# Optimization experiments

Measured on AMD Instinct MI355X. Metric: run time of the kernel, lower is better.

Reference implementation:

```python
import jax, jax.numpy as jnp
import numpy as np

N_KNOTS = 8
LATENT = 16
DEGREE = 3


def _de_boor(x, t, c, p):
    # x: arbitrary-shape query points; t: (n_knots+6,) padded knots; c: (n_knots+2,) control points
    k = jnp.digitize(x, t) - 1  # interval index per element (binary search gather)
    d = [c[k + (j - p)] for j in range(p + 1)]
    for r in range(1, p + 1):
        for j in range(p, r - 1, -1):
            t_lo = t[k + (j - p)]
            t_hi = t[k + (j + 1 - r)]
            alpha = (x - t_lo) / (t_hi - t_lo)
            d[j] = (1.0 - alpha) * d[j - 1] + alpha * d[j]
    return d[p]


def setup_inputs() -> dict:
    key = jax.random.key(0)
    ks = jax.random.split(key, 8)
    # |k| grid normalized to fftfreq range: values in [0, sqrt(3)]
    x = jax.random.uniform(ks[0], (256, 256, 256), dtype=jnp.float32) * 1.7320508
    a = jax.random.uniform(ks[1], (1,), dtype=jnp.float32)  # scale factor in (0,1)
    inv = 1.0 / np.sqrt(LATENT).astype(np.float32)
    W1 = jax.random.normal(ks[2], (1, LATENT), jnp.float32)
    b1 = jnp.zeros((LATENT,), jnp.float32)
    W2 = jax.random.normal(ks[3], (LATENT, LATENT), jnp.float32) * inv
    b2 = jnp.zeros((LATENT,), jnp.float32)
    Ww = jax.random.normal(ks[4], (LATENT, N_KNOTS + 1), jnp.float32) * inv
    bw = jnp.zeros((N_KNOTS + 1,), jnp.float32)
    Wk = jax.random.normal(ks[5], (LATENT, N_KNOTS - 1), jnp.float32) * inv
    bk = jnp.zeros((N_KNOTS - 1,), jnp.float32)
    return {"x": x, "a": a, "W1": W1, "b1": b1, "W2": W2, "b2": b2,
            "Ww": Ww, "bw": bw, "Wk": Wk, "bk": bk}


def reference(x, a, W1, b1, W2, b2, Ww, bw, Wk, bk):
    # tiny MLP on scalar a -> spline weights w and knot increments k
    net = jnp.sin(a @ W1 + b1)           # (LATENT,)
    net = jnp.sin(net @ W2 + b2)         # (LATENT,)
    w = net @ Ww + bw                    # (N_KNOTS+1,)
    kk = net @ Wk + bk                   # (N_KNOTS-1,)
    kk = jnp.concatenate([jnp.zeros((1,), x.dtype), jnp.cumsum(jax.nn.softmax(kk))])  # (N_KNOTS,), monotone in [0,1]
    w = jnp.concatenate([jnp.zeros((1,), x.dtype), w])                                 # (N_KNOTS+2,)
    ak = jnp.concatenate([jnp.zeros((3,), x.dtype), kk, jnp.ones((3,), x.dtype)])      # padded knots
    xq = jnp.clip(x / jnp.sqrt(jnp.asarray(3.0, x.dtype)), 0.0, 1.0 - 0.0001)
    return _de_boor(xq, ak, w, DEGREE)
```

## Files before the change

kernel.cpp:

```cpp
#include <hip/hip_runtime.h>
#include <math.h>

typedef float f4 __attribute__((ext_vector_type(4)));

__device__ __forceinline__ float eval_one(float xv,
                                          float c1, float c2, float c3,
                                          float k1, float k2, float k3,
                                          float k4, float k5, float k6,
                                          float e1, float e2, float e3,
                                          float e4, float e5, float e6)
{
    const float xq = fminf(fmaxf(xv * 0.57735026918962576f, 0.0f), 0.9999f);
    float acc = xq * fmaf(fmaf(c3, xq, c2), xq, c1);
    float r;
    r = fmaxf(xq - k1, 0.f); acc = fmaf(e1 * r, r * r, acc);
    r = fmaxf(xq - k2, 0.f); acc = fmaf(e2 * r, r * r, acc);
    r = fmaxf(xq - k3, 0.f); acc = fmaf(e3 * r, r * r, acc);
    r = fmaxf(xq - k4, 0.f); acc = fmaf(e4 * r, r * r, acc);
    r = fmaxf(xq - k5, 0.f); acc = fmaf(e5 * r, r * r, acc);
    r = fmaxf(xq - k6, 0.f); acc = fmaf(e6 * r, r * r, acc);
    return acc;
}

__global__ __launch_bounds__(256) void nsf_fused2_kernel(
    const float* __restrict__ x,
    const float* __restrict__ a,
    const float* __restrict__ W1, const float* __restrict__ b1,
    const float* __restrict__ W2, const float* __restrict__ b2,
    const float* __restrict__ Ww, const float* __restrict__ bw,
    const float* __restrict__ Wk, const float* __restrict__ bk,
    float* __restrict__ out, int n)
{
    const int n4 = n >> 2;
    const int gid = blockIdx.x * blockDim.x + threadIdx.x;
    const int stride = gridDim.x * blockDim.x;
    const f4* __restrict__ x4 = reinterpret_cast<const f4*>(x);
    f4* __restrict__ o4 = reinterpret_cast<f4*>(out);

    const int j16 = threadIdx.x & 15;

    const float av  = a[0];
    const float w1v = W1[j16];
    const float b1v = b1[j16];
    const float b2v = b2[j16];
    float w2l[16];
#pragma unroll
    for (int i = 0; i < 16; ++i) w2l[i] = W2[i * 16 + j16];
    const bool isw = (j16 < 9);
    const float* hW = isw ? (Ww + j16) : (Wk + (j16 - 9));
    const int hs = isw ? 9 : 7;
    const float hbv = isw ? bw[j16] : bk[j16 - 9];
    float hl[16];
#pragma unroll
    for (int i = 0; i < 16; ++i) hl[i] = hW[i * hs];

    f4 v[8];
#pragma unroll
    for (int it = 0; it < 8; ++it) {
        const int idx = gid + it * stride;
        if (idx < n4) v[it] = __builtin_nontemporal_load(x4 + idx);
    }

    const float n1own = __sinf(fmaf(av, w1v, b1v));
    float s2 = b2v;
#pragma unroll
    for (int i = 0; i < 16; ++i)
        s2 = fmaf(__shfl(n1own, i, 64), w2l[i], s2);
    const float n2own = __sinf(s2);

    float hsum = hbv;
#pragma unroll
    for (int i = 0; i < 16; ++i)
        hsum = fmaf(__shfl(n2own, i, 64), hl[i], hsum);

    float hv[16];
#pragma unroll
    for (int i = 0; i < 16; ++i) hv[i] = __shfl(hsum, i, 64);

    float m = hv[9];
#pragma unroll
    for (int j = 1; j < 7; ++j) m = fmaxf(m, hv[9 + j]);
    float ex[7], se = 0.f;
#pragma unroll
    for (int j = 0; j < 7; ++j) { ex[j] = __expf(hv[9 + j] - m); se += ex[j]; }
    const float sinv = __builtin_amdgcn_rcpf(se);

    float t[14];
    t[0] = t[1] = t[2] = t[3] = 0.f;
    {
        float cum = 0.f;
#pragma unroll
        for (int j = 0; j < 7; ++j) { cum += ex[j] * sinv; t[4 + j] = cum; }
    }
    t[11] = t[12] = t[13] = 1.f;

    float cc[10];
    cc[0] = 0.f;
#pragma unroll
    for (int j = 0; j < 9; ++j) cc[1 + j] = hv[j];

    float c1v[10];
#pragma unroll
    for (int i = 1; i < 10; ++i)
        c1v[i] = 3.f * (cc[i] - cc[i - 1]) * __builtin_amdgcn_rcpf(t[i + 3] - t[i]);
    float c2v[10];
#pragma unroll
    for (int i = 2; i < 10; ++i)
        c2v[i] = 2.f * (c1v[i] - c1v[i - 1]) * __builtin_amdgcn_rcpf(t[i + 2] - t[i]);
    float c3v[10];
#pragma unroll
    for (int i = 3; i < 10; ++i)
        c3v[i] = (c2v[i] - c2v[i - 1]) * __builtin_amdgcn_rcpf(t[i + 1] - t[i]);

    const float p0c1 = c1v[1];
    const float p0c2 = c2v[2] * 0.5f;
    const float p0c3 = c3v[3] * (1.f / 6.f);

    const float k1 = t[4], k2 = t[5], k3 = t[6], k4 = t[7], k5 = t[8], k6 = t[9];
    const float e1 = (c3v[4] - c3v[3]) * (1.f / 6.f);
    const float e2 = (c3v[5] - c3v[4]) * (1.f / 6.f);
    const float e3 = (c3v[6] - c3v[5]) * (1.f / 6.f);
    const float e4 = (c3v[7] - c3v[6]) * (1.f / 6.f);
    const float e5 = (c3v[8] - c3v[7]) * (1.f / 6.f);
    const float e6 = (c3v[9] - c3v[8]) * (1.f / 6.f);

#pragma unroll
    for (int it = 0; it < 8; ++it) {
        const int idx = gid + it * stride;
        if (idx < n4) {
            f4 r;
            r.x = eval_one(v[it].x, p0c1,p0c2,p0c3, k1,k2,k3,k4,k5,k6, e1,e2,e3,e4,e5,e6);
            r.y = eval_one(v[it].y, p0c1,p0c2,p0c3, k1,k2,k3,k4,k5,k6, e1,e2,e3,e4,e5,e6);
            r.z = eval_one(v[it].z, p0c1,p0c2,p0c3, k1,k2,k3,k4,k5,k6, e1,e2,e3,e4,e5,e6);
            r.w = eval_one(v[it].w, p0c1,p0c2,p0c3, k1,k2,k3,k4,k5,k6, e1,e2,e3,e4,e5,e6);
            __builtin_nontemporal_store(r, o4 + idx);
        }
    }
    for (int idx = gid + 8 * stride; idx < n4; idx += stride) {
        const f4 vv = x4[idx];
        f4 r;
        r.x = eval_one(vv.x, p0c1,p0c2,p0c3, k1,k2,k3,k4,k5,k6, e1,e2,e3,e4,e5,e6);
        r.y = eval_one(vv.y, p0c1,p0c2,p0c3, k1,k2,k3,k4,k5,k6, e1,e2,e3,e4,e5,e6);
        r.z = eval_one(vv.z, p0c1,p0c2,p0c3, k1,k2,k3,k4,k5,k6, e1,e2,e3,e4,e5,e6);
        r.w = eval_one(vv.w, p0c1,p0c2,p0c3, k1,k2,k3,k4,k5,k6, e1,e2,e3,e4,e5,e6);
        o4[idx] = r;
    }
    for (int j = (n4 << 2) + gid; j < n; j += stride)
        out[j] = eval_one(x[j], p0c1,p0c2,p0c3, k1,k2,k3,k4,k5,k6, e1,e2,e3,e4,e5,e6);
}

extern "C" void kernel_launch(void* const* d_in, const int* in_sizes, int n_in,
                              void* d_out, int out_size, void* d_ws, size_t ws_size,
                              hipStream_t stream)
{
    const float* x  = (const float*)d_in[0];
    const float* a  = (const float*)d_in[1];
    const float* W1 = (const float*)d_in[2];
    const float* b1 = (const float*)d_in[3];
    const float* W2 = (const float*)d_in[4];
    const float* b2 = (const float*)d_in[5];
    const float* Ww = (const float*)d_in[6];
    const float* bw = (const float*)d_in[7];
    const float* Wk = (const float*)d_in[8];
    const float* bk = (const float*)d_in[9];
    float* out = (float*)d_out;
    const int n = out_size;

    const int n4 = n >> 2;
    int blocks = (n4 + 256 * 8 - 1) / (256 * 8);
    if (blocks < 1) blocks = 1;

    hipLaunchKernelGGL(nsf_fused2_kernel, dim3(blocks), dim3(256), 0, stream,
                       x, a, W1, b1, W2, b2, Ww, bw, Wk, bk, out, n);
}
```

Baseline: 141.2 us.

## Use readlane broadcasts for MLP coefficients and drop register prefetch of inputs

Swaps the __shfl cross-lane broadcasts (LDS-based bpermute) for readlane/readfirstlane so the spline coefficients become wave-uniform scalar values, which lowers VGPR pressure. It also removes the 8-deep register prefetch of x that overlapped the load with the MLP prologue, and replaces the unrolled batch with a plain grid-stride loop using nontemporal stores. The cost is that load latency is no longer hidden behind the coefficient computation, and each thread now issues its f4 loads one at a time inside the loop.

```diff
diff --git a/kernel.cpp b/kernel.cpp
--- a/kernel.cpp
+++ b/kernel.cpp
@@ -2,6 +2,13 @@
 #include <math.h>
 
 typedef float f4 __attribute__((ext_vector_type(4)));
+
+__device__ __forceinline__ float rdlane(float v, int l) {
+    return __int_as_float(__builtin_amdgcn_readlane(__float_as_int(v), l));
+}
+__device__ __forceinline__ float rdfirst(float v) {
+    return __int_as_float(__builtin_amdgcn_readfirstlane(__float_as_int(v)));
+}
 
 __device__ __forceinline__ float eval_one(float xv,
                                           float c1, float c2, float c3,
@@ -22,7 +29,7 @@
     return acc;
 }
 
-__global__ __launch_bounds__(256) void nsf_fused2_kernel(
+__global__ __launch_bounds__(256) void nsf_fused3_kernel(
     const float* __restrict__ x,
     const float* __restrict__ a,
     const float* __restrict__ W1, const float* __restrict__ b1,
@@ -31,51 +38,26 @@
     const float* __restrict__ Wk, const float* __restrict__ bk,
     float* __restrict__ out, int n)
 {
-    const int n4 = n >> 2;
-    const int gid = blockIdx.x * blockDim.x + threadIdx.x;
-    const int stride = gridDim.x * blockDim.x;
-    const f4* __restrict__ x4 = reinterpret_cast<const f4*>(x);
-    f4* __restrict__ o4 = reinterpret_cast<f4*>(out);
-
     const int j16 = threadIdx.x & 15;
 
-    const float av  = a[0];
-    const float w1v = W1[j16];
-    const float b1v = b1[j16];
-    const float b2v = b2[j16];
-    float w2l[16];
-#pragma unroll
-    for (int i = 0; i < 16; ++i) w2l[i] = W2[i * 16 + j16];
-    const bool isw = (j16 < 9);
-    const float* hW = isw ? (Ww + j16) : (Wk + (j16 - 9));
-    const int hs = isw ? 9 : 7;
-    const float hbv = isw ? bw[j16] : bk[j16 - 9];
-    float hl[16];
-#pragma unroll
-    for (int i = 0; i < 16; ++i) hl[i] = hW[i * hs];
-
-    f4 v[8];
-#pragma unroll
-    for (int it = 0; it < 8; ++it) {
-        const int idx = gid + it * stride;
-        if (idx < n4) v[it] = __builtin_nontemporal_load(x4 + idx);
-    }
-
-    const float n1own = __sinf(fmaf(av, w1v, b1v));
-    float s2 = b2v;
+    const float n1own = __sinf(fmaf(a[0], W1[j16], b1[j16]));
+    float s2 = b2[j16];
 #pragma unroll
     for (int i = 0; i < 16; ++i)
-        s2 = fmaf(__shfl(n1own, i, 64), w2l[i], s2);
+        s2 = fmaf(rdlane(n1own, i), W2[i * 16 + j16], s2);
     const float n2own = __sinf(s2);
 
-    float hsum = hbv;
+    const bool isw = (j16 < 9);
+    const float* hp = isw ? (Ww + j16) : (Wk + (j16 - 9));
+    const int hs = isw ? 9 : 7;
+    float hsum = isw ? bw[j16] : bk[j16 - 9];
 #pragma unroll
     for (int i = 0; i < 16; ++i)
-        hsum = fmaf(__shfl(n2own, i, 64), hl[i], hsum);
+        hsum = fmaf(rdlane(n2own, i), hp[i * hs], hsum);
 
     float hv[16];
 #pragma unroll
-    for (int i = 0; i < 16; ++i) hv[i] = __shfl(hsum, i, 64);
+    for (int i = 0; i < 16; ++i) hv[i] = rdlane(hsum, i);
 
     float m = hv[9];
 #pragma unroll
@@ -112,38 +94,32 @@
     for (int i = 3; i < 10; ++i)
         c3v[i] = (c2v[i] - c2v[i - 1]) * __builtin_amdgcn_rcpf(t[i + 1] - t[i]);
 
-    const float p0c1 = c1v[1];
-    const float p0c2 = c2v[2] * 0.5f;
-    const float p0c3 = c3v[3] * (1.f / 6.f);
+    const float p0c1 = rdfirst(c1v[1]);
+    const float p0c2 = rdfirst(c2v[2] * 0.5f);
+    const float p0c3 = rdfirst(c3v[3] * (1.f / 6.f));
+    const float k1 = rdfirst(t[4]), k2 = rdfirst(t[5]), k3 = rdfirst(t[6]);
+    const float k4 = rdfirst(t[7]), k5 = rdfirst(t[8]), k6 = rdfirst(t[9]);
+    const float e1 = rdfirst((c3v[4] - c3v[3]) * (1.f / 6.f));
+    const float e2 = rdfirst((c3v[5] - c3v[4]) * (1.f / 6.f));
+    const float e3 = rdfirst((c3v[6] - c3v[5]) * (1.f / 6.f));
+    const float e4 = rdfirst((c3v[7] - c3v[6]) * (1.f / 6.f));
+    const float e5 = rdfirst((c3v[8] - c3v[7]) * (1.f / 6.f));
+    const float e6 = rdfirst((c3v[9] - c3v[8]) * (1.f / 6.f));
 
-    const float k1 = t[4], k2 = t[5], k3 = t[6], k4 = t[7], k5 = t[8], k6 = t[9];
-    const float e1 = (c3v[4] - c3v[3]) * (1.f / 6.f);
-    const float e2 = (c3v[5] - c3v[4]) * (1.f / 6.f);
-    const float e3 = (c3v[6] - c3v[5]) * (1.f / 6.f);
-    const float e4 = (c3v[7] - c3v[6]) * (1.f / 6.f);
-    const float e5 = (c3v[8] - c3v[7]) * (1.f / 6.f);
-    const float e6 = (c3v[9] - c3v[8]) * (1.f / 6.f);
+    const int n4 = n >> 2;
+    const int gid = blockIdx.x * blockDim.x + threadIdx.x;
+    const int stride = gridDim.x * blockDim.x;
+    const f4* __restrict__ x4 = reinterpret_cast<const f4*>(x);
+    f4* __restrict__ o4 = reinterpret_cast<f4*>(out);
 
-#pragma unroll
-    for (int it = 0; it < 8; ++it) {
-        const int idx = gid + it * stride;
-        if (idx < n4) {
-            f4 r;
-            r.x = eval_one(v[it].x, p0c1,p0c2,p0c3, k1,k2,k3,k4,k5,k6, e1,e2,e3,e4,e5,e6);
-            r.y = eval_one(v[it].y, p0c1,p0c2,p0c3, k1,k2,k3,k4,k5,k6, e1,e2,e3,e4,e5,e6);
-            r.z = eval_one(v[it].z, p0c1,p0c2,p0c3, k1,k2,k3,k4,k5,k6, e1,e2,e3,e4,e5,e6);
-            r.w = eval_one(v[it].w, p0c1,p0c2,p0c3, k1,k2,k3,k4,k5,k6, e1,e2,e3,e4,e5,e6);
-            __builtin_nontemporal_store(r, o4 + idx);
-        }
-    }
-    for (int idx = gid + 8 * stride; idx < n4; idx += stride) {
-        const f4 vv = x4[idx];
+    for (int idx = gid; idx < n4; idx += stride) {
+        const f4 v = x4[idx];
         f4 r;
-        r.x = eval_one(vv.x, p0c1,p0c2,p0c3, k1,k2,k3,k4,k5,k6, e1,e2,e3,e4,e5,e6);
-        r.y = eval_one(vv.y, p0c1,p0c2,p0c3, k1,k2,k3,k4,k5,k6, e1,e2,e3,e4,e5,e6);
-        r.z = eval_one(vv.z, p0c1,p0c2,p0c3, k1,k2,k3,k4,k5,k6, e1,e2,e3,e4,e5,e6);
-        r.w = eval_one(vv.w, p0c1,p0c2,p0c3, k1,k2,k3,k4,k5,k6, e1,e2,e3,e4,e5,e6);
-        o4[idx] = r;
+        r.x = eval_one(v.x, p0c1,p0c2,p0c3, k1,k2,k3,k4,k5,k6, e1,e2,e3,e4,e5,e6);
+        r.y = eval_one(v.y, p0c1,p0c2,p0c3, k1,k2,k3,k4,k5,k6, e1,e2,e3,e4,e5,e6);
+        r.z = eval_one(v.z, p0c1,p0c2,p0c3, k1,k2,k3,k4,k5,k6, e1,e2,e3,e4,e5,e6);
+        r.w = eval_one(v.w, p0c1,p0c2,p0c3, k1,k2,k3,k4,k5,k6, e1,e2,e3,e4,e5,e6);
+        __builtin_nontemporal_store(r, o4 + idx);
     }
     for (int j = (n4 << 2) + gid; j < n; j += stride)
         out[j] = eval_one(x[j], p0c1,p0c2,p0c3, k1,k2,k3,k4,k5,k6, e1,e2,e3,e4,e5,e6);
@@ -170,6 +146,6 @@
     int blocks = (n4 + 256 * 8 - 1) / (256 * 8);
     if (blocks < 1) blocks = 1;
 
-    hipLaunchKernelGGL(nsf_fused2_kernel, dim3(blocks), dim3(256), 0, stream,
+    hipLaunchKernelGGL(nsf_fused3_kernel, dim3(blocks), dim3(256), 0, stream,
                        x, a, W1, b1, W2, b2, Ww, bw, Wk, bk, out, n);
 }
```

After: 128.4 us. 1.1x faster.
